# Kernel optimization log

Measured on AMD Instinct MI355X. Metric: run time of the kernel, lower is better.

The kernel has to match this reference:

```python
import jax, jax.numpy as jnp
import numpy as np

HEADS = 4
DIM_HEAD = 64
QUERY_DIM = 512
CONTEXT_DIM = 512
INNER = HEADS * DIM_HEAD  # 256
SCALE = DIM_HEAD ** -0.5


def setup_inputs() -> dict:
    key = jax.random.key(0)
    ks = jax.random.split(key, 9)
    b, n, m = 4, 2048, 2048
    inp = {
        'x1': jax.random.normal(ks[0], (b, n, QUERY_DIM), jnp.float32),
        'x2': jax.random.normal(ks[1], (b, n, QUERY_DIM), jnp.float32),
        'context': jax.random.normal(ks[2], (b, m, CONTEXT_DIM), jnp.float32),
        # weights stored [in, out] (= torch weight.T)
        'Wq': jax.random.normal(ks[3], (QUERY_DIM, INNER), jnp.float32) * (QUERY_DIM ** -0.5),
        'Wq2': jax.random.normal(ks[4], (QUERY_DIM, INNER), jnp.float32) * (QUERY_DIM ** -0.5),
        'Wk': jax.random.normal(ks[5], (CONTEXT_DIM, INNER), jnp.float32) * (CONTEXT_DIM ** -0.5),
        'Wv': jax.random.normal(ks[6], (CONTEXT_DIM, INNER), jnp.float32) * (CONTEXT_DIM ** -0.5),
        'Wo': jax.random.normal(ks[7], (INNER, QUERY_DIM), jnp.float32) * (INNER ** -0.5),
        'bo': jax.random.normal(ks[8], (QUERY_DIM,), jnp.float32) * 0.01,
    }
    return inp


def _split_heads(t):
    # [b, n, h*d] -> [b, h, n, d]
    b, n, _ = t.shape
    return t.reshape(b, n, HEADS, DIM_HEAD).transpose(0, 2, 1, 3)


def reference(x1, x2, context, Wq, Wq2, Wk, Wv, Wo, bo):
    q = _split_heads(x1 @ Wq)
    q2 = _split_heads(x2 @ Wq2)
    k = _split_heads(context @ Wk)
    v = _split_heads(context @ Wv)
    sim = jnp.einsum('bhid,bhjd->bhij', q, k) * SCALE
    sim2 = jnp.einsum('bhid,bhjd->bhij', q2, k) * SCALE
    attn = 0.3 * jax.nn.softmax(sim, axis=-1) + 0.7 * jax.nn.softmax(sim2, axis=-1)
    out = jnp.einsum('bhij,bhjd->bhid', attn, v)  # [b, h, n, d]
    b, h, n, d = out.shape
    out = out.transpose(0, 2, 1, 3).reshape(b, n, h * d)
    return out @ Wo + bo
```

## Files before the change

kernel.cpp:

```cpp
#include <hip/hip_runtime.h>

typedef __attribute__((ext_vector_type(8))) short bf16x8;
typedef __attribute__((ext_vector_type(4))) float f32x4;
typedef unsigned short ushort_t;
typedef unsigned int uint_t;

__device__ __forceinline__ ushort_t f2bf(float f) {
    unsigned int x = __builtin_bit_cast(unsigned int, f);
    x += 0x7fffu + ((x >> 16) & 1u);
    return (ushort_t)(x >> 16);
}
__device__ __forceinline__ uint_t pack2_rn(float a, float b) {
    uint_t au = __builtin_bit_cast(uint_t, a) + 0x8000u;
    uint_t bu = __builtin_bit_cast(uint_t, b) + 0x8000u;
    return __builtin_amdgcn_perm(bu, au, 0x07060302);
}

#define LOG2E 1.4426950408889634f

#define WT_OFF   0
#define WOT_OFF  524288
#define QKV_OFF  655360
#define QKV_SZ   2097152
#define QKV_OFF_Z3 (3 * (size_t)QKV_SZ)
#define O_OFF    9043968

__global__ __launch_bounds__(256) void transpose_w(
    const float* __restrict__ Wq, const float* __restrict__ Wq2,
    const float* __restrict__ Wk, const float* __restrict__ Wv,
    const float* __restrict__ Wo, ushort_t* __restrict__ ws)
{
    const int j = blockIdx.y;
    const int t = blockIdx.x * 256 + threadIdx.x;
    const float* in;
    ushort_t* out;
    int W;
    if (j < 4) {
        in = (j == 0) ? Wq : (j == 1) ? Wq2 : (j == 2) ? Wk : Wv;
        out = ws + WT_OFF + (size_t)j * 131072;
        W = 512;
    } else {
        in = Wo; out = ws + WOT_OFF; W = 256;
    }
    const int Cin = 131072 / W;
    const float s = (j < 2) ? (0.125f * LOG2E) : 1.0f;
    out[t] = f2bf(in[(size_t)(t % W) * Cin + (t / W)] * s);
}

__global__ __launch_bounds__(256) void proj_gemm(
    const float* __restrict__ x1, const float* __restrict__ x2,
    const float* __restrict__ ctx, const ushort_t* __restrict__ Wt,
    ushort_t* __restrict__ QKV)
{
    __shared__ __align__(16) ushort_t lA[64 * 40];
    __shared__ __align__(16) ushort_t lB[256 * 40];
    const int z = blockIdx.y;
    const float* A = (z == 0) ? x1 : (z == 1) ? x2 : ctx;
    const ushort_t* Bt = Wt + (size_t)z * 131072;
    const int tid = threadIdx.x;
    const int wave = tid >> 6, lane = tid & 63;
    const int quad = lane >> 4, l16 = lane & 15;
    const size_t row0 = (size_t)blockIdx.x * 64;
    const int sr = tid >> 2, sc8 = (tid & 3) << 3;

    f32x4 acc[16] = {};
    for (int k0 = 0; k0 < 512; k0 += 32) {
        const float* src = A + (row0 + sr) * 512 + k0 + sc8;
        float4 v0 = *(const float4*)src;
        float4 v1 = *(const float4*)(src + 4);
        uint4 packed;
        packed.x = pack2_rn(v0.x, v0.y);
        packed.y = pack2_rn(v0.z, v0.w);
        packed.z = pack2_rn(v1.x, v1.y);
        packed.w = pack2_rn(v1.z, v1.w);
        *(uint4*)&lA[sr * 40 + sc8] = packed;
#pragma unroll
        for (int rr = 0; rr < 4; ++rr)
            *(uint4*)&lB[(rr * 64 + sr) * 40 + sc8] =
                *(const uint4*)(Bt + (size_t)(rr * 64 + sr) * 512 + k0 + sc8);
        __syncthreads();
        bf16x8 af = *(const bf16x8*)&lA[(wave * 16 + l16) * 40 + quad * 8];
        if (z == 3) {
#pragma unroll
            for (int c = 0; c < 16; ++c) {
                bf16x8 bfr = *(const bf16x8*)&lB[(c * 16 + l16) * 40 + quad * 8];
                acc[c] = __builtin_amdgcn_mfma_f32_16x16x32_bf16(af, bfr, acc[c], 0, 0, 0);
            }
        } else {
#pragma unroll
            for (int c = 0; c < 16; ++c) {
                bf16x8 bfr = *(const bf16x8*)&lB[(c * 16 + l16) * 40 + quad * 8];
                acc[c] = __builtin_amdgcn_mfma_f32_16x16x32_bf16(bfr, af, acc[c], 0, 0, 0);
            }
        }
        __syncthreads();
    }
    if (z == 3) {
        const int b = (int)(row0 >> 11);
        const int tokl = ((int)row0 & 2047) + wave * 16 + quad * 4;
        ushort_t* Vt = QKV + QKV_OFF_Z3;
#pragma unroll
        for (int c = 0; c < 16; ++c) {
            const int col = c * 16 + l16;
            const int h = col >> 6, d = col & 63;
            uint2 w;
            w.x = pack2_rn(acc[c][0], acc[c][1]);
            w.y = pack2_rn(acc[c][2], acc[c][3]);
            *(uint2*)(Vt + ((size_t)((b * 4 + h) * 64 + d)) * 2048 + tokl) = w;
        }
    } else {
        ushort_t* C = QKV + (size_t)z * QKV_SZ;
        const size_t tok = row0 + wave * 16 + l16;
#pragma unroll
        for (int c = 0; c < 16; ++c) {
            uint2 w;
            w.x = pack2_rn(acc[c][0], acc[c][1]);
            w.y = pack2_rn(acc[c][2], acc[c][3]);
            *(uint2*)(C + tok * 256 + c * 16 + quad * 4) = w;
        }
    }
}

__global__ __launch_bounds__(256) void out_gemm(
    const ushort_t* __restrict__ Op, const ushort_t* __restrict__ Wot,
    const float* __restrict__ bias, float* __restrict__ out)
{
    __shared__ __align__(16) ushort_t lA[64 * 40];
    __shared__ __align__(16) ushort_t lB[256 * 40];
    const int tid = threadIdx.x;
    const int wave = tid >> 6, lane = tid & 63;
    const int quad = lane >> 4, l16 = lane & 15;
    const size_t row0 = (size_t)blockIdx.x * 64;
    const int col0 = blockIdx.y * 256;
    const int sr = tid >> 2, sc8 = (tid & 3) << 3;

    f32x4 acc[16] = {};
    for (int k0 = 0; k0 < 256; k0 += 32) {
        *(uint4*)&lA[sr * 40 + sc8] = *(const uint4*)(Op + (row0 + sr) * 256 + k0 + sc8);
#pragma unroll
        for (int rr = 0; rr < 4; ++rr)
            *(uint4*)&lB[(rr * 64 + sr) * 40 + sc8] =
                *(const uint4*)(Wot + (size_t)(col0 + rr * 64 + sr) * 256 + k0 + sc8);
        __syncthreads();
        bf16x8 af = *(const bf16x8*)&lA[(wave * 16 + l16) * 40 + quad * 8];
#pragma unroll
        for (int c = 0; c < 16; ++c) {
            bf16x8 bfr = *(const bf16x8*)&lB[(c * 16 + l16) * 40 + quad * 8];
            acc[c] = __builtin_amdgcn_mfma_f32_16x16x32_bf16(bfr, af, acc[c], 0, 0, 0);
        }
        __syncthreads();
    }
    const size_t tok = row0 + wave * 16 + l16;
#pragma unroll
    for (int c = 0; c < 16; ++c) {
        const int col = col0 + c * 16 + quad * 4;
        const float4 bv = *(const float4*)&bias[col];
        float4 o;
        o.x = acc[c][0] + bv.x; o.y = acc[c][1] + bv.y;
        o.z = acc[c][2] + bv.z; o.w = acc[c][3] + bv.w;
        *(float4*)&out[tok * 512 + col] = o;
    }
}


#define ATTN_STAGE(MB, BUF) do {                                                        \
    _Pragma("unroll")                                                                   \
    for (int it_ = 0; it_ < 2; ++it_) {                                                 \
        const int cc_ = tid + it_ * 256;                                                \
        const int g_ = (cc_ ^ (cc_ >> 3)) & 7;                                          \
        const ushort_t* kp_ = Kb + (size_t)(tok0 + (MB) + (cc_ >> 3)) * 256 + in0 + g_ * 8; \
        __builtin_amdgcn_global_load_lds(                                               \
            (const __attribute__((address_space(1))) void*)kp_,                         \
            (__attribute__((address_space(3))) void*)&lK[BUF][cc_ * 8], 16, 0, 0);      \
        const ushort_t* vp_ = Vt + (size_t)(bh64 + (cc_ >> 3)) * 2048 + (MB) + g_ * 8;  \
        __builtin_amdgcn_global_load_lds(                                               \
            (const __attribute__((address_space(1))) void*)vp_,                         \
            (__attribute__((address_space(3))) void*)&lV[BUF][cc_ * 8], 16, 0, 0);      \
    }                                                                                   \
} while (0)

#define ATTN_ITER(I, P) do {                                                            \
    __syncthreads();                                                                    \
    { const int mn_ = ((I) + 1) * 64; if (mn_ < 2048) ATTN_STAGE(mn_, 1 - (P)); }       \
    f32x4 st1[4] = {}, st2[4] = {};                                                     \
    _Pragma("unroll")                                                                   \
    for (int c = 0; c < 4; ++c) {                                                       \
        _Pragma("unroll")                                                               \
        for (int ks = 0; ks < 2; ++ks) {                                                \
            bf16x8 kf = *(const bf16x8*)&lK[P][(c * 16 + l16) * 64 +                    \
                                              ((((ks * 4 + quad) ^ l7) & 7) << 3)];     \
            st1[c] = __builtin_amdgcn_mfma_f32_16x16x32_bf16(kf, q1f[ks], st1[c], 0, 0, 0); \
            st2[c] = __builtin_amdgcn_mfma_f32_16x16x32_bf16(kf, q2f[ks], st2[c], 0, 0, 0); \
        } }                                                                             \
    _Pragma("unroll")                                                                   \
    for (int c = 0; c < 4; ++c) {                                                       \
        float p0 = __builtin_amdgcn_exp2f(st1[c][0]);                                   \
        float p1 = __builtin_amdgcn_exp2f(st1[c][1]);                                   \
        float p2 = __builtin_amdgcn_exp2f(st1[c][2]);                                   \
        float p3 = __builtin_amdgcn_exp2f(st1[c][3]);                                   \
        l1 += (p0 + p1) + (p2 + p3);                                                    \
        uint2 w; w.x = pack2_rn(p0, p1); w.y = pack2_rn(p2, p3);                        \
        *(uint2*)&lPw0[l16 * 72 + c * 16 + quad * 4] = w;                               \
        float r0 = __builtin_amdgcn_exp2f(st2[c][0]);                                   \
        float r1 = __builtin_amdgcn_exp2f(st2[c][1]);                                   \
        float r2 = __builtin_amdgcn_exp2f(st2[c][2]);                                   \
        float r3 = __builtin_amdgcn_exp2f(st2[c][3]);                                   \
        l2 += (r0 + r1) + (r2 + r3);                                                    \
        uint2 y; y.x = pack2_rn(r0, r1); y.y = pack2_rn(r2, r3);                        \
        *(uint2*)&lPw1[l16 * 72 + c * 16 + quad * 4] = y;                               \
    }                                                                                   \
    bf16x8 pa1[2], pa2[2];                                                              \
    _Pragma("unroll")                                                                   \
    for (int ks = 0; ks < 2; ++ks) {                                                    \
        pa1[ks] = *(const bf16x8*)&lPw0[l16 * 72 + ks * 32 + quad * 8];                 \
        pa2[ks] = *(const bf16x8*)&lPw1[l16 * 72 + ks * 32 + quad * 8];                 \
    }                                                                                   \
    _Pragma("unroll")                                                                   \
    for (int c = 0; c < 4; ++c) {                                                       \
        _Pragma("unroll")                                                               \
        for (int ks = 0; ks < 2; ++ks) {                                                \
            bf16x8 vf = *(const bf16x8*)&lV[P][(c * 16 + l16) * 64 +                    \
                                              ((((ks * 4 + quad) ^ l7) & 7) << 3)];     \
            o1[c] = __builtin_amdgcn_mfma_f32_16x16x32_bf16(vf, pa1[ks], o1[c], 0, 0, 0); \
            o2[c] = __builtin_amdgcn_mfma_f32_16x16x32_bf16(vf, pa2[ks], o2[c], 0, 0, 0); \
        } }                                                                             \
} while (0)

__global__ __launch_bounds__(256) void attn_fused(
    const ushort_t* __restrict__ Qb, const ushort_t* __restrict__ Q2b,
    const ushort_t* __restrict__ Kb, const ushort_t* __restrict__ Vt,
    ushort_t* __restrict__ Ob)
{
    __shared__ __align__(16) ushort_t lK[2][64 * 64];
    __shared__ __align__(16) ushort_t lV[2][64 * 64];
    __shared__ __align__(16) ushort_t lP[4][2][16 * 72];

    const int qt = blockIdx.x;
    const int bh = blockIdx.y;
    const int tid = threadIdx.x;
    const int wave = tid >> 6, lane = tid & 63;
    const int quad = lane >> 4, l16 = lane & 15;
    const int l7 = l16 & 7;
    const size_t tok0 = (size_t)(bh >> 2) * 2048;
    const int in0 = (bh & 3) * 64;
    const int bh64 = bh * 64;
    ushort_t* lPw0 = &lP[wave][0][0];
    ushort_t* lPw1 = &lP[wave][1][0];

    bf16x8 q1f[2], q2f[2];
    {
        const ushort_t* qr1 = Qb  + (tok0 + qt * 64 + wave * 16 + l16) * 256 + in0;
        const ushort_t* qr2 = Q2b + (tok0 + qt * 64 + wave * 16 + l16) * 256 + in0;
#pragma unroll
        for (int ks = 0; ks < 2; ++ks) {
            q1f[ks] = *(const bf16x8*)(qr1 + ks * 32 + quad * 8);
            q2f[ks] = *(const bf16x8*)(qr2 + ks * 32 + quad * 8);
        }
    }

    ATTN_STAGE(0, 0);

    f32x4 o1[4] = {}, o2[4] = {};
    float l1 = 0.f, l2 = 0.f;

    for (int i = 0; i < 32; i += 2) {
        ATTN_ITER(i, 0);
        ATTN_ITER(i + 1, 1);
    }

    l1 += __shfl_xor(l1, 16, 64); l1 += __shfl_xor(l1, 32, 64);
    l2 += __shfl_xor(l2, 16, 64); l2 += __shfl_xor(l2, 32, 64);
    const float inv1 = 0.3f / l1, inv2 = 0.7f / l2;

    ushort_t* orow = Ob + (tok0 + qt * 64 + wave * 16 + l16) * 256 + in0;
#pragma unroll
    for (int c = 0; c < 4; ++c) {
        const float f0 = o1[c][0] * inv1 + o2[c][0] * inv2;
        const float f1 = o1[c][1] * inv1 + o2[c][1] * inv2;
        const float f2 = o1[c][2] * inv1 + o2[c][2] * inv2;
        const float f3 = o1[c][3] * inv1 + o2[c][3] * inv2;
        uint2 w; w.x = pack2_rn(f0, f1); w.y = pack2_rn(f2, f3);
        *(uint2*)(orow + c * 16 + quad * 4) = w;
    }
}

extern "C" void kernel_launch(void* const* d_in, const int* in_sizes, int n_in,
                              void* d_out, int out_size, void* d_ws, size_t ws_size,
                              hipStream_t stream)
{
    (void)in_sizes; (void)n_in; (void)out_size; (void)ws_size;
    const float* x1  = (const float*)d_in[0];
    const float* x2  = (const float*)d_in[1];
    const float* ctx = (const float*)d_in[2];
    const float* Wq  = (const float*)d_in[3];
    const float* Wq2 = (const float*)d_in[4];
    const float* Wk  = (const float*)d_in[5];
    const float* Wv  = (const float*)d_in[6];
    const float* Wo  = (const float*)d_in[7];
    const float* bo  = (const float*)d_in[8];
    ushort_t* ws  = (ushort_t*)d_ws;
    float* out = (float*)d_out;

    ushort_t* Wt  = ws + WT_OFF;
    ushort_t* Wot = ws + WOT_OFF;
    ushort_t* QKV = ws + QKV_OFF;
    ushort_t* Q   = QKV;
    ushort_t* Q2  = QKV + 1 * (size_t)QKV_SZ;
    ushort_t* Kp  = QKV + 2 * (size_t)QKV_SZ;
    ushort_t* Vt  = QKV + 3 * (size_t)QKV_SZ;
    ushort_t* Op  = ws + O_OFF;

    transpose_w<<<dim3(512, 5), 256, 0, stream>>>(Wq, Wq2, Wk, Wv, Wo, ws);
    proj_gemm  <<<dim3(128, 4), 256, 0, stream>>>(x1, x2, ctx, Wt, QKV);
    attn_fused <<<dim3(32, 16), 256, 0, stream>>>(Q, Q2, Kp, Vt, Op);
    out_gemm   <<<dim3(128, 2), 256, 0, stream>>>(Op, Wot, bo, out);
}
```

Before: 203.5 us.

## Tile weight transpose through LDS and serialize dual-softmax P buffers in attention

The weight transpose kernel now stages 64x64 tiles in shared memory, so both the global reads and the writes are coalesced instead of strided scalar gathers. In the attention loop, the two probability tiles now share one swizzled per-wave LDS buffer. Each softmax branch is written, read back and multiplied by V before the next, which cuts LDS use and live registers. The kernel also gains a launch bound of 4 blocks per CU to push occupancy up. The trade-off is less overlap between the two branches and a dependency chain through the shared P buffer.

Result: slower. 259.5 us (+27.5%).

```diff
diff --git a/kernel.cpp b/kernel.cpp
--- a/kernel.cpp
+++ b/kernel.cpp
@@ -30,21 +30,35 @@
     const float* __restrict__ Wk, const float* __restrict__ Wv,
     const float* __restrict__ Wo, ushort_t* __restrict__ ws)
 {
-    const int j = blockIdx.y;
-    const int t = blockIdx.x * 256 + threadIdx.x;
+    const int z = blockIdx.z;
     const float* in;
-    ushort_t* out;
-    int W;
-    if (j < 4) {
-        in = (j == 0) ? Wq : (j == 1) ? Wq2 : (j == 2) ? Wk : Wv;
-        out = ws + WT_OFF + (size_t)j * 131072;
-        W = 512;
+    ushort_t* outp;
+    int R, C;
+    float s = 1.0f;
+    if (z < 4) {
+        in = (z == 0) ? Wq : (z == 1) ? Wq2 : (z == 2) ? Wk : Wv;
+        outp = ws + WT_OFF + (size_t)z * 131072;
+        R = 512; C = 256;
+        if (z < 2) s = 0.125f * LOG2E;
     } else {
-        in = Wo; out = ws + WOT_OFF; W = 256;
-    }
-    const int Cin = 131072 / W;
-    const float s = (j < 2) ? (0.125f * LOG2E) : 1.0f;
-    out[t] = f2bf(in[(size_t)(t % W) * Cin + (t / W)] * s);
+        in = Wo; outp = ws + WOT_OFF; R = 256; C = 512;
+    }
+    const int rt = blockIdx.x * 64, ct = blockIdx.y * 64;
+    if (rt >= R || ct >= C) return;
+    __shared__ float lT[64][65];
+    const int tid = threadIdx.x;
+    const int ci = tid & 63, ri0 = tid >> 6;
+#pragma unroll
+    for (int it = 0; it < 16; ++it) {
+        const int r = ri0 + it * 4;
+        lT[r][ci] = in[(size_t)(rt + r) * C + ct + ci];
+    }
+    __syncthreads();
+#pragma unroll
+    for (int it = 0; it < 16; ++it) {
+        const int orow = ri0 + it * 4;
+        outp[(size_t)(ct + orow) * R + rt + ci] = f2bf(lT[ci][orow] * s);
+    }
 }
 
 __global__ __launch_bounds__(256) void proj_gemm(
@@ -179,6 +193,31 @@
     }                                                                                   \
 } while (0)
 
+#define P_WRITE(ST, LS) do {                                                            \
+    _Pragma("unroll")                                                                   \
+    for (int c = 0; c < 4; ++c) {                                                       \
+        float p0 = __builtin_amdgcn_exp2f(ST[c][0]);                                    \
+        float p1 = __builtin_amdgcn_exp2f(ST[c][1]);                                    \
+        float p2 = __builtin_amdgcn_exp2f(ST[c][2]);                                    \
+        float p3 = __builtin_amdgcn_exp2f(ST[c][3]);                                    \
+        LS += (p0 + p1) + (p2 + p3);                                                    \
+        uint2 w; w.x = pack2_rn(p0, p1); w.y = pack2_rn(p2, p3);                        \
+        *(uint2*)&lPw[l16 * 64 + ((((c * 2 + (quad >> 1)) ^ l7) & 7) << 3) +            \
+                      ((quad & 1) << 2)] = w;                                           \
+    }                                                                                   \
+} while (0)
+
+#define PV_MFMA(OA, PAV, P) do {                                                        \
+    _Pragma("unroll")                                                                   \
+    for (int c = 0; c < 4; ++c) {                                                       \
+        _Pragma("unroll")                                                               \
+        for (int ks = 0; ks < 2; ++ks) {                                                \
+            bf16x8 vf = *(const bf16x8*)&lV[P][(c * 16 + l16) * 64 +                    \
+                                              ((((ks * 4 + quad) ^ l7) & 7) << 3)];     \
+            OA[c] = __builtin_amdgcn_mfma_f32_16x16x32_bf16(vf, PAV[ks], OA[c], 0, 0, 0); \
+        } }                                                                             \
+} while (0)
+
 #define ATTN_ITER(I, P) do {                                                            \
     __syncthreads();                                                                    \
     { const int mn_ = ((I) + 1) * 64; if (mn_ < 2048) ATTN_STAGE(mn_, 1 - (P)); }       \
@@ -192,48 +231,27 @@
             st1[c] = __builtin_amdgcn_mfma_f32_16x16x32_bf16(kf, q1f[ks], st1[c], 0, 0, 0); \
             st2[c] = __builtin_amdgcn_mfma_f32_16x16x32_bf16(kf, q2f[ks], st2[c], 0, 0, 0); \
         } }                                                                             \
-    _Pragma("unroll")                                                                   \
-    for (int c = 0; c < 4; ++c) {                                                       \
-        float p0 = __builtin_amdgcn_exp2f(st1[c][0]);                                   \
-        float p1 = __builtin_amdgcn_exp2f(st1[c][1]);                                   \
-        float p2 = __builtin_amdgcn_exp2f(st1[c][2]);                                   \
-        float p3 = __builtin_amdgcn_exp2f(st1[c][3]);                                   \
-        l1 += (p0 + p1) + (p2 + p3);                                                    \
-        uint2 w; w.x = pack2_rn(p0, p1); w.y = pack2_rn(p2, p3);                        \
-        *(uint2*)&lPw0[l16 * 72 + c * 16 + quad * 4] = w;                               \
-        float r0 = __builtin_amdgcn_exp2f(st2[c][0]);                                   \
-        float r1 = __builtin_amdgcn_exp2f(st2[c][1]);                                   \
-        float r2 = __builtin_amdgcn_exp2f(st2[c][2]);                                   \
-        float r3 = __builtin_amdgcn_exp2f(st2[c][3]);                                   \
-        l2 += (r0 + r1) + (r2 + r3);                                                    \
-        uint2 y; y.x = pack2_rn(r0, r1); y.y = pack2_rn(r2, r3);                        \
-        *(uint2*)&lPw1[l16 * 72 + c * 16 + quad * 4] = y;                               \
-    }                                                                                   \
-    bf16x8 pa1[2], pa2[2];                                                              \
-    _Pragma("unroll")                                                                   \
-    for (int ks = 0; ks < 2; ++ks) {                                                    \
-        pa1[ks] = *(const bf16x8*)&lPw0[l16 * 72 + ks * 32 + quad * 8];                 \
-        pa2[ks] = *(const bf16x8*)&lPw1[l16 * 72 + ks * 32 + quad * 8];                 \
-    }                                                                                   \
-    _Pragma("unroll")                                                                   \
-    for (int c = 0; c < 4; ++c) {                                                       \
-        _Pragma("unroll")                                                               \
-        for (int ks = 0; ks < 2; ++ks) {                                                \
-            bf16x8 vf = *(const bf16x8*)&lV[P][(c * 16 + l16) * 64 +                    \
-                                              ((((ks * 4 + quad) ^ l7) & 7) << 3)];     \
-            o1[c] = __builtin_amdgcn_mfma_f32_16x16x32_bf16(vf, pa1[ks], o1[c], 0, 0, 0); \
-            o2[c] = __builtin_amdgcn_mfma_f32_16x16x32_bf16(vf, pa2[ks], o2[c], 0, 0, 0); \
-        } }                                                                             \
+    P_WRITE(st1, l1);                                                                   \
+    bf16x8 pa[2];                                                                       \
+    _Pragma("unroll")                                                                   \
+    for (int ks = 0; ks < 2; ++ks)                                                      \
+        pa[ks] = *(const bf16x8*)&lPw[l16 * 64 + ((((ks * 4 + quad) ^ l7) & 7) << 3)];  \
+    PV_MFMA(o1, pa, P);                                                                 \
+    P_WRITE(st2, l2);                                                                   \
+    _Pragma("unroll")                                                                   \
+    for (int ks = 0; ks < 2; ++ks)                                                      \
+        pa[ks] = *(const bf16x8*)&lPw[l16 * 64 + ((((ks * 4 + quad) ^ l7) & 7) << 3)];  \
+    PV_MFMA(o2, pa, P);                                                                 \
 } while (0)
 
-__global__ __launch_bounds__(256) void attn_fused(
+__global__ __launch_bounds__(256, 4) void attn_fused(
     const ushort_t* __restrict__ Qb, const ushort_t* __restrict__ Q2b,
     const ushort_t* __restrict__ Kb, const ushort_t* __restrict__ Vt,
     ushort_t* __restrict__ Ob)
 {
     __shared__ __align__(16) ushort_t lK[2][64 * 64];
     __shared__ __align__(16) ushort_t lV[2][64 * 64];
-    __shared__ __align__(16) ushort_t lP[4][2][16 * 72];
+    __shared__ __align__(16) ushort_t lP[4][16 * 64];
 
     const int qt = blockIdx.x;
     const int bh = blockIdx.y;
@@ -244,8 +262,7 @@
     const size_t tok0 = (size_t)(bh >> 2) * 2048;
     const int in0 = (bh & 3) * 64;
     const int bh64 = bh * 64;
-    ushort_t* lPw0 = &lP[wave][0][0];
-    ushort_t* lPw1 = &lP[wave][1][0];
+    ushort_t* lPw = &lP[wave][0];
 
     bf16x8 q1f[2], q2f[2];
     {
@@ -310,7 +327,7 @@
     ushort_t* Vt  = QKV + 3 * (size_t)QKV_SZ;
     ushort_t* Op  = ws + O_OFF;
 
-    transpose_w<<<dim3(512, 5), 256, 0, stream>>>(Wq, Wq2, Wk, Wv, Wo, ws);
+    transpose_w<<<dim3(8, 8, 5), 256, 0, stream>>>(Wq, Wq2, Wk, Wv, Wo, ws);
     proj_gemm  <<<dim3(128, 4), 256, 0, stream>>>(x1, x2, ctx, Wt, QKV);
     attn_fused <<<dim3(32, 16), 256, 0, stream>>>(Q, Q2, Kp, Vt, Op);
     out_gemm   <<<dim3(128, 2), 256, 0, stream>>>(Op, Wot, bo, out);
```
